# Kernel tuning notes

Hardware: AMD Instinct MI355X
Metric: run time of the kernel (lower is better)

Reference implementation:

```python
import jax, jax.numpy as jnp
import numpy as np

D_MODEL = 1024
DK = 64
H = D_MODEL // DK
EPS = 1e-5


def setup_inputs() -> dict:
    key = jax.random.key(0)
    ks = jax.random.split(key, 8)
    B, M = 4, 2048
    s = 1.0 / np.sqrt(D_MODEL)
    return {
        "inp": jax.random.normal(ks[0], (B, M, D_MODEL), dtype=jnp.float32),
        "Wq": jax.random.normal(ks[1], (D_MODEL, D_MODEL), dtype=jnp.float32) * s,
        "bq": jnp.zeros((D_MODEL,), dtype=jnp.float32),
        "Wk": jax.random.normal(ks[2], (D_MODEL, D_MODEL), dtype=jnp.float32) * s,
        "bk": jnp.zeros((D_MODEL,), dtype=jnp.float32),
        "Wv": jax.random.normal(ks[3], (D_MODEL, D_MODEL), dtype=jnp.float32) * s,
        "bv": jnp.zeros((D_MODEL,), dtype=jnp.float32),
        "gamma": jnp.ones((D_MODEL,), dtype=jnp.float32),
        "beta": jnp.zeros((D_MODEL,), dtype=jnp.float32),
    }


def reference(inp, Wq, bq, Wk, bk, Wv, bv, gamma, beta):
    B, M, _ = inp.shape
    # LayerNorm over last dim
    mu = jnp.mean(inp, axis=-1, keepdims=True)
    var = jnp.mean(jnp.square(inp - mu), axis=-1, keepdims=True)
    out = (inp - mu) * jax.lax.rsqrt(var + EPS) * gamma + beta
    # QKV projections (x @ W + b)
    Q = (out @ Wq + bq).reshape(B, M, DK, H)
    K = (out @ Wk + bk).reshape(B, M, DK, H)
    V = (out @ Wv + bv).reshape(B, M, DK, H)
    # per-position attention over the dk axis, contracting h
    scores = jnp.einsum("bmih,bmjh->bmij", Q, K) / np.sqrt(DK)  # [B,M,dk,dk]
    att = jax.nn.softmax(scores, axis=-1)
    res = jnp.einsum("bmij,bmjh->bmih", att, V).reshape(B, M, D_MODEL)
    # dropout is identity at eval; positionals add in original is dead code
    return inp + res
```

## Files before the change

### kernel.cpp

```cpp
#include <hip/hip_runtime.h>
#include <hip/hip_bf16.h>

#define D_MODEL 1024
#define NQKV 3072

typedef __attribute__((ext_vector_type(8))) short bf16x8;
typedef __attribute__((ext_vector_type(4))) float f32x4;
typedef __attribute__((ext_vector_type(16))) float f32x16;
typedef __attribute__((ext_vector_type(8))) unsigned short u16x8;

static __device__ __forceinline__ unsigned short f2bf(float f){
  unsigned int x = __float_as_uint(f);
  x += 0x7fff + ((x >> 16) & 1);
  return (unsigned short)(x >> 16);
}
static __device__ __forceinline__ float bf2f(unsigned short u){
  return __uint_as_float(((unsigned int)u) << 16);
}

__global__ __launch_bounds__(256) void fused_pre_kernel(const float* __restrict__ inp,
    const float* __restrict__ gamma, const float* __restrict__ beta,
    const float* __restrict__ Wq, const float* __restrict__ Wk,
    const float* __restrict__ Wv, const float* __restrict__ bq,
    const float* __restrict__ bk, const float* __restrict__ bv,
    unsigned short* __restrict__ X, unsigned short* __restrict__ Wt,
    float* __restrict__ bc){
  if (blockIdx.x < 8192){
    const int row = blockIdx.x;
    const int t = threadIdx.x;
    const float4* ip = (const float4*)(inp + (size_t)row * D_MODEL);
    float4 v = ip[t];
    float s1 = v.x + v.y + v.z + v.w;
    float s2 = v.x*v.x + v.y*v.y + v.z*v.z + v.w*v.w;
#pragma unroll
    for (int off = 32; off >= 1; off >>= 1){
      s1 += __shfl_down(s1, off);
      s2 += __shfl_down(s2, off);
    }
    __shared__ float red[8];
    const int wave = t >> 6, lane = t & 63;
    if (lane == 0){ red[wave] = s1; red[4 + wave] = s2; }
    __syncthreads();
    s1 = red[0] + red[1] + red[2] + red[3];
    s2 = red[4] + red[5] + red[6] + red[7];
    const float mu   = s1 * (1.0f / D_MODEL);
    const float var  = s2 * (1.0f / D_MODEL) - mu * mu;
    const float rstd = rsqrtf(var + 1e-5f);
    float4 g = ((const float4*)gamma)[t];
    float4 b = ((const float4*)beta)[t];
    ushort4 o;
    o.x = f2bf((v.x - mu) * rstd * g.x + b.x);
    o.y = f2bf((v.y - mu) * rstd * g.y + b.y);
    o.z = f2bf((v.z - mu) * rstd * g.z + b.z);
    o.w = f2bf((v.w - mu) * rstd * g.w + b.w);
    ((ushort4*)(X + (size_t)row * D_MODEL))[t] = o;
  } else {
    __shared__ float tile[32][33];
    const int idx = blockIdx.x - 8192;
    const int kx = idx & 31, ny = (idx >> 5) & 31, z = idx >> 10;
    const float* W = (z == 0) ? Wq : ((z == 1) ? Wk : Wv);
    const int k0 = kx * 32, n0 = ny * 32;
    const int r = threadIdx.x >> 5, c = threadIdx.x & 31;
    if (kx == 0 && r == 0){
      const float* bsrc = (z == 0) ? bq : ((z == 1) ? bk : bv);
      bc[z * 1024 + n0 + c] = bsrc[n0 + c];
    }
#pragma unroll
    for (int i = 0; i < 4; i++)
      tile[r + i*8][c] = W[(size_t)(k0 + r + i*8) * D_MODEL + n0 + c];
    __syncthreads();
    unsigned short* dst = Wt + (size_t)(z * D_MODEL + n0) * D_MODEL + k0;
#pragma unroll
    for (int i = 0; i < 4; i++){
      int rr = r + i*8;
      dst[(size_t)rr * D_MODEL + c] = f2bf(tile[c][rr]);
    }
  }
}


#define GLL(src, dst) __builtin_amdgcn_global_load_lds( \
    (const __attribute__((address_space(1))) void*)(src), \
    (__attribute__((address_space(3))) void*)(dst), 16, 0, 0)

#define STAGE(tsrc, bi) do { \
  const char* _sa = Ag + (size_t)r0*2048 + (size_t)(tsrc)*128 + co; \
  char* _da = ldsS + (size_t)(bi)*49152 + tid*16; \
  GLL(_sa, _da); GLL(_sa + 131072, _da + 8192); \
  const char* _sb = Bg + (size_t)r0*2048 + (size_t)(tsrc)*128 + co; \
  char* _db = ldsS + (size_t)(bi)*49152 + 16384 + tid*16; \
  GLL(_sb, _db); GLL(_sb + 131072, _db + 8192); \
  GLL(_sb + 262144, _db + 16384); GLL(_sb + 393216, _db + 24576); \
} while(0)

#define BODY(bi) do { \
  const char* Ab = ldsS + (size_t)(bi)*49152 + (wr*64 + lr)*128; \
  const char* Bb = ldsS + (size_t)(bi)*49152 + 16384 + (wc*64 + lr)*128; \
  bf16x8 Ar[4][2], Br[4][2]; \
  _Pragma("unroll") \
  for (int m = 0; m < 4; m++){ \
    Ar[m][0] = *(const bf16x8*)(Ab + m*2048 + colb0); \
    Ar[m][1] = *(const bf16x8*)(Ab + m*2048 + colb1); \
  } \
  _Pragma("unroll") \
  for (int n = 0; n < 4; n++){ \
    Br[n][0] = *(const bf16x8*)(Bb + n*2048 + colb0); \
    Br[n][1] = *(const bf16x8*)(Bb + n*2048 + colb1); \
  } \
  _Pragma("unroll") \
  for (int m = 0; m < 4; m++) \
    _Pragma("unroll") \
    for (int n = 0; n < 4; n++){ \
      acc[m][n] = __builtin_amdgcn_mfma_f32_16x16x32_bf16(Ar[m][0], Br[n][0], acc[m][n], 0, 0, 0); \
      acc[m][n] = __builtin_amdgcn_mfma_f32_16x16x32_bf16(Ar[m][1], Br[n][1], acc[m][n], 0, 0, 0); \
    } \
} while(0)

#define BARRIER __builtin_amdgcn_s_barrier()
#define SCHEDB  __builtin_amdgcn_sched_barrier(0)
#define VMCNT6  asm volatile("s_waitcnt vmcnt(6)" ::: "memory")
#define VMCNT0  asm volatile("s_waitcnt vmcnt(0)" ::: "memory")

__global__ __launch_bounds__(512, 2) void gemm128x256_kernel(const unsigned short* __restrict__ A,
    const unsigned short* __restrict__ Bt, const float* __restrict__ bias,
    unsigned short* __restrict__ C){
  __shared__ __align__(16) char ldsS[3 * 49152];
  const int tid = threadIdx.x;
  const int wave = tid >> 6, lane = tid & 63;
  const int wr = wave >> 2, wc = wave & 3;
  const int lr = lane & 15;
  const int colb0 = ((lane >> 4) * 16) ^ ((lane & 7) << 4);
  const int colb1 = (64 + (lane >> 4) * 16) ^ ((lane & 7) << 4);

  const int b = blockIdx.x;
  const int xcd = b & 7;
  const int i = b >> 3;
  const int mi = i & 7, ni = i >> 3;
  const int m0 = (xcd * 8 + mi) * 128;
  const int n0 = ni * 256;

  const int r0 = tid >> 3;
  const size_t co = (size_t)(((tid & 7) * 16) ^ ((r0 & 7) << 4));
  const char* Ag = (const char*)(A + (size_t)m0 * 1024);
  const char* Bg = (const char*)(Bt + (size_t)n0 * 1024);

  f32x4 acc[4][4] = {};

  STAGE(0, 0);
  STAGE(1, 1);
  VMCNT6; BARRIER; SCHEDB;

  for (int t = 0; t < 16; ++t){
    if (t <= 13) STAGE(t + 2, (t + 2) % 3);
    BODY(t % 3);
    if (t <= 13)      { SCHEDB; VMCNT6; BARRIER; SCHEDB; }
    else if (t == 14) { SCHEDB; VMCNT0; BARRIER; SCHEDB; }
  }

  const int gm = m0 + wr*64;
  const int gn = n0 + wc*64;
  const int rr0 = (lane >> 4) * 4;
#pragma unroll
  for (int nf = 0; nf < 4; nf++){
    const int gcol = gn + nf*16 + lr;
    const float bb = bias[gcol];
#pragma unroll
    for (int mf = 0; mf < 4; mf++){
      const int grow = gm + mf*16 + rr0;
#pragma unroll
      for (int r = 0; r < 4; r++)
        C[(size_t)(grow + r) * NQKV + gcol] = f2bf(acc[mf][nf][r] + bb);
    }
  }
}

__global__ __launch_bounds__(256) void attn_kernel(const unsigned short* __restrict__ qkv,
    const float* __restrict__ inp, float* __restrict__ out){
  __shared__ unsigned short P[4][64 * 64];
  const int wave = threadIdx.x >> 6, lane = threadIdx.x & 63;
  const int token = blockIdx.x * 4 + wave;
  const unsigned short* row = qkv + (size_t)token * NQKV;
  const int l31 = lane & 31, hi = lane >> 5;
  const int l15 = lane & 15, qg = lane >> 4;
  char* pbase = (char*)&P[wave][0];

  bf16x8 kf[2], qf[2];
#pragma unroll
  for (int mt = 0; mt < 2; mt++)
    kf[mt] = *(const bf16x8*)(row + 1024 + (mt*32 + l31)*16 + hi*8);
#pragma unroll
  for (int nt = 0; nt < 2; nt++)
    qf[nt] = *(const bf16x8*)(row + (nt*32 + l31)*16 + hi*8);

  bf16x8 vf[2];
#pragma unroll
  for (int kc = 0; kc < 2; kc++)
#pragma unroll
    for (int e = 0; e < 8; e++)
      vf[kc][e] = (short)row[2048 + (kc*32 + qg*8 + e)*16 + l15];

  f32x16 s[2][2] = {};
#pragma unroll
  for (int mt = 0; mt < 2; mt++)
#pragma unroll
    for (int nt = 0; nt < 2; nt++)
      s[mt][nt] = __builtin_amdgcn_mfma_f32_32x32x16_bf16(kf[mt], qf[nt], s[mt][nt], 0, 0, 0);

#pragma unroll
  for (int ti = 0; ti < 2; ti++){
    float m = s[0][ti][0];
#pragma unroll
    for (int mt = 0; mt < 2; mt++)
#pragma unroll
      for (int r = 0; r < 16; r++) m = fmaxf(m, s[mt][ti][r]);
    m = fmaxf(m, __shfl_xor(m, 32));
    float sum = 0.0f;
#pragma unroll
    for (int mt = 0; mt < 2; mt++)
#pragma unroll
      for (int r = 0; r < 16; r++){
        float p = exp2f((s[mt][ti][r] - m) * 0.1803368801f);
        s[mt][ti][r] = p;
        sum += p;
      }
    sum += __shfl_xor(sum, 32);
    const float invs = 1.0f / sum;
    const int i = ti*32 + l31;
    const int sw = (i & 7) << 4;
#pragma unroll
    for (int mt = 0; mt < 2; mt++)
#pragma unroll
      for (int g = 0; g < 4; g++){
        ushort4 pk;
        pk.x = f2bf(s[mt][ti][4*g + 0] * invs);
        pk.y = f2bf(s[mt][ti][4*g + 1] * invs);
        pk.z = f2bf(s[mt][ti][4*g + 2] * invs);
        pk.w = f2bf(s[mt][ti][4*g + 3] * invs);
        const int jbyte = mt*64 + g*16 + hi*8;
        *(ushort4*)(pbase + ((i*128 + jbyte) ^ sw)) = pk;
      }
  }
  __syncthreads();

  f32x4 o[4] = {};
#pragma unroll
  for (int nt = 0; nt < 4; nt++){
    const int n = nt*16 + l15;
    const int swr = (n & 7) << 4;
#pragma unroll
    for (int kc = 0; kc < 2; kc++){
      bf16x8 pb = *(const bf16x8*)(pbase + ((n*128 + kc*64 + qg*16) ^ swr));
      o[nt] = __builtin_amdgcn_mfma_f32_16x16x32_bf16(vf[kc], pb, o[nt], 0, 0, 0);
    }
  }

  const size_t base = (size_t)token * D_MODEL;
#pragma unroll
  for (int nt = 0; nt < 4; nt++){
    const int i = nt*16 + l15;
    const float4 iv = *(const float4*)(inp + base + i*16 + qg*4);
    float4 ov;
    ov.x = iv.x + o[nt][0];
    ov.y = iv.y + o[nt][1];
    ov.z = iv.z + o[nt][2];
    ov.w = iv.w + o[nt][3];
    *(float4*)(out + base + i*16 + qg*4) = ov;
  }
}

extern "C" void kernel_launch(void* const* d_in, const int* in_sizes, int n_in,
                              void* d_out, int out_size, void* d_ws, size_t ws_size,
                              hipStream_t stream) {
  const float* inp   = (const float*)d_in[0];
  const float* Wq    = (const float*)d_in[1];
  const float* bq    = (const float*)d_in[2];
  const float* Wk    = (const float*)d_in[3];
  const float* bk    = (const float*)d_in[4];
  const float* Wv    = (const float*)d_in[5];
  const float* bv    = (const float*)d_in[6];
  const float* gamma = (const float*)d_in[7];
  const float* beta  = (const float*)d_in[8];
  float* out = (float*)d_out;

  char* ws = (char*)d_ws;
  unsigned short* Xln  = (unsigned short*)ws;
  unsigned short* Wt   = (unsigned short*)(ws + 16777216);
  float*          bc   = (float*)(ws + 23068672);
  unsigned short* QKV  = (unsigned short*)(ws + 23080960);

  fused_pre_kernel<<<11264, 256, 0, stream>>>(inp, gamma, beta, Wq, Wk, Wv,
                                              bq, bk, bv, Xln, Wt, bc);
  gemm128x256_kernel<<<768, 512, 0, stream>>>(Xln, Wt, bc, QKV);
  attn_kernel<<<2048, 256, 0, stream>>>(QKV, inp, out);
}
```

Measured before the change: 94.13 us.

## Make QKV GEMM persistent over three N tiles with cross-tile prefetch

The GEMM launch drops from 768 to 256 blocks, and each block now computes three 128x256 output tiles that share the same A rows and sit 1024 columns apart. The triple-buffered load pipeline keeps running across tile boundaries, so the first K-slices of the next tile are prefetched while the current one finishes. This is meant to remove the pipeline fill and drain per tile and to improve reuse of the A rows. In exchange, 256 blocks at two per CU may leave some of the 256 CUs' slots idle and reduce occupancy-based latency hiding, and the epilogue stores are serialized inside each block.

```diff
diff --git a/kernel.cpp b/kernel.cpp
--- a/kernel.cpp
+++ b/kernel.cpp
@@ -83,11 +83,11 @@
     (const __attribute__((address_space(1))) void*)(src), \
     (__attribute__((address_space(3))) void*)(dst), 16, 0, 0)
 
-#define STAGE(tsrc, bi) do { \
-  const char* _sa = Ag + (size_t)r0*2048 + (size_t)(tsrc)*128 + co; \
+#define STAGE2(AG, BG, tsrc, bi) do { \
+  const char* _sa = (AG) + (size_t)r0*2048 + (size_t)(tsrc)*128 + co; \
   char* _da = ldsS + (size_t)(bi)*49152 + tid*16; \
   GLL(_sa, _da); GLL(_sa + 131072, _da + 8192); \
-  const char* _sb = Bg + (size_t)r0*2048 + (size_t)(tsrc)*128 + co; \
+  const char* _sb = (BG) + (size_t)r0*2048 + (size_t)(tsrc)*128 + co; \
   char* _db = ldsS + (size_t)(bi)*49152 + 16384 + tid*16; \
   GLL(_sb, _db); GLL(_sb + 131072, _db + 8192); \
   GLL(_sb + 262144, _db + 16384); GLL(_sb + 393216, _db + 24576); \
@@ -121,7 +121,7 @@
 #define VMCNT6  asm volatile("s_waitcnt vmcnt(6)" ::: "memory")
 #define VMCNT0  asm volatile("s_waitcnt vmcnt(0)" ::: "memory")
 
-__global__ __launch_bounds__(512, 2) void gemm128x256_kernel(const unsigned short* __restrict__ A,
+__global__ __launch_bounds__(512, 2) void gemm_pers_kernel(const unsigned short* __restrict__ A,
     const unsigned short* __restrict__ Bt, const float* __restrict__ bias,
     unsigned short* __restrict__ C){
   __shared__ __align__(16) char ldsS[3 * 49152];
@@ -134,42 +134,61 @@
 
   const int b = blockIdx.x;
   const int xcd = b & 7;
-  const int i = b >> 3;
-  const int mi = i & 7, ni = i >> 3;
+  const int j = b >> 3;
+  const int mi = j & 7;
+  const int ni0 = j >> 3;
   const int m0 = (xcd * 8 + mi) * 128;
-  const int n0 = ni * 256;
+  const int n00 = ni0 * 256;
 
   const int r0 = tid >> 3;
   const size_t co = (size_t)(((tid & 7) * 16) ^ ((r0 & 7) << 4));
-  const char* Ag = (const char*)(A + (size_t)m0 * 1024);
-  const char* Bg = (const char*)(Bt + (size_t)n0 * 1024);
+  const char* Ag  = (const char*)(A + (size_t)m0 * 1024);
+  const char* Bg0 = (const char*)(Bt + (size_t)n00 * 1024);
 
   f32x4 acc[4][4] = {};
 
-  STAGE(0, 0);
-  STAGE(1, 1);
+  STAGE2(Ag, Bg0, 0, 0);
+  STAGE2(Ag, Bg0, 1, 1);
   VMCNT6; BARRIER; SCHEDB;
 
-  for (int t = 0; t < 16; ++t){
-    if (t <= 13) STAGE(t + 2, (t + 2) % 3);
-    BODY(t % 3);
-    if (t <= 13)      { SCHEDB; VMCNT6; BARRIER; SCHEDB; }
-    else if (t == 14) { SCHEDB; VMCNT0; BARRIER; SCHEDB; }
-  }
-
-  const int gm = m0 + wr*64;
-  const int gn = n0 + wc*64;
-  const int rr0 = (lane >> 4) * 4;
-#pragma unroll
-  for (int nf = 0; nf < 4; nf++){
-    const int gcol = gn + nf*16 + lr;
-    const float bb = bias[gcol];
-#pragma unroll
-    for (int mf = 0; mf < 4; mf++){
-      const int grow = gm + mf*16 + rr0;
-#pragma unroll
-      for (int r = 0; r < 4; r++)
-        C[(size_t)(grow + r) * NQKV + gcol] = f2bf(acc[mf][nf][r] + bb);
+#pragma unroll
+  for (int p = 0; p < 3; ++p){
+    const char* Bp  = Bg0 + (size_t)p * 2097152;
+    const char* Bp1 = Bg0 + (size_t)(p + 1) * 2097152;
+    for (int t = 0; t < 16; ++t){
+      if (t <= 13)     STAGE2(Ag, Bp,  t + 2,  (p + t + 2) % 3);
+      else if (p < 2)  STAGE2(Ag, Bp1, t - 14, (p + t + 2) % 3);
+      BODY((p + t) % 3);
+      if (p < 2){
+        SCHEDB; VMCNT6; BARRIER; SCHEDB;
+      } else {
+        if (t <= 13)      { SCHEDB; VMCNT6; BARRIER; SCHEDB; }
+        else if (t == 14) { SCHEDB; VMCNT0; BARRIER; SCHEDB; }
+      }
+    }
+    {
+      const int gm = m0 + wr * 64;
+      const int gn = n00 + p * 1024 + wc * 64;
+      const int rr0 = (lane >> 4) * 4;
+#pragma unroll
+      for (int nf = 0; nf < 4; nf++){
+        const int gcol = gn + nf*16 + lr;
+        const float bb = bias[gcol];
+#pragma unroll
+        for (int mf = 0; mf < 4; mf++){
+          const int grow = gm + mf*16 + rr0;
+#pragma unroll
+          for (int r = 0; r < 4; r++)
+            C[(size_t)(grow + r) * NQKV + gcol] = f2bf(acc[mf][nf][r] + bb);
+        }
+      }
+    }
+    if (p < 2){
+#pragma unroll
+      for (int m = 0; m < 4; m++)
+#pragma unroll
+        for (int n = 0; n < 4; n++)
+          acc[m][n] = (f32x4){0.0f, 0.0f, 0.0f, 0.0f};
     }
   }
 }
@@ -290,6 +309,6 @@
 
   fused_pre_kernel<<<11264, 256, 0, stream>>>(inp, gamma, beta, Wq, Wk, Wv,
                                               bq, bk, bv, Xln, Wt, bc);
-  gemm128x256_kernel<<<768, 512, 0, stream>>>(Xln, Wt, bc, QKV);
+  gemm_pers_kernel<<<256, 512, 0, stream>>>(Xln, Wt, bc, QKV);
   attn_kernel<<<2048, 256, 0, stream>>>(QKV, inp, out);
 }
```

Measured after the change: 92.07 us. -2.2%, faster.
